# Performance work log

Hardware: AMD Instinct MI355X
Metric: run time of the kernel (lower is better)

## Reference

```python
import jax, jax.numpy as jnp
import numpy as np

N, K, C_IN, H, W = 32, 17, 2048, 64, 64
POSEMB, HID, NLAYERS = 64, 128, 4
IMG = jnp.array([1920.0, 1080.0, 1920.0, 1080.0], jnp.float32)  # image_width/height from img_metas
# H36M 17-joint skeleton edges
EDGES = [(0,1),(1,2),(2,3),(0,4),(4,5),(5,6),(0,7),(7,8),(8,9),(9,10),(8,11),(11,12),(12,13),(8,14),(14,15),(15,16)]
_m = np.eye(K, dtype=bool)
for _i, _j in EDGES:
    _m[_i, _j] = _m[_j, _i] = True
ADJ_MASK = jnp.asarray(_m)
EYE = jnp.eye(K, dtype=jnp.float32)
BN_EPS = 1e-5


def semgconv(x, Wp, b, E):
    # SemGraphConv: separate weights for self (W[0]) and neighbor (W[1]) paths,
    # learned edge logits E masked to the skeleton and row-softmaxed.
    h0 = jnp.einsum('bkc,cd->bkd', x, Wp[0])
    h1 = jnp.einsum('bkc,cd->bkd', x, Wp[1])
    adj = jax.nn.softmax(jnp.where(ADJ_MASK, E, -9e15), axis=1)
    return (jnp.einsum('ij,bjd->bid', adj * EYE, h0)
            + jnp.einsum('ij,bjd->bid', adj * (1.0 - EYE), h1) + b)


def bn_relu(x, gamma, beta):
    # BatchNorm1d in eval mode with running_mean=0, running_var=1, then ReLU.
    return jax.nn.relu(x * gamma * jax.lax.rsqrt(jnp.float32(1.0 + BN_EPS)) + beta)


def setup_inputs() -> dict:
    key = jax.random.key(0)
    ks = jax.random.split(key, 12)
    C_emb = POSEMB + C_IN  # 2112
    NG = 2 * NLAYERS       # 8 hidden graph convs (4 residual blocks x 2)
    return {
        'x': jax.random.normal(ks[0], (N, C_IN, H, W), jnp.float32),
        'heatmap': jax.random.uniform(ks[1], (N, K, H, W), jnp.float32),
        'bbox': jax.random.uniform(ks[2], (N, 4), jnp.float32) * IMG,
        'pos_w': jax.random.normal(ks[3], (6, POSEMB), jnp.float32) * 0.2,
        'pos_b': jnp.zeros((POSEMB,), jnp.float32),
        'Wi': jax.random.normal(ks[4], (2, C_emb, HID), jnp.float32) * 0.02,
        'bi': jnp.zeros((HID,), jnp.float32),
        'Ei': jax.random.normal(ks[5], (K, K), jnp.float32),
        'gi': jnp.ones((HID,), jnp.float32),
        'bti': jnp.zeros((HID,), jnp.float32),
        'Wh': jax.random.normal(ks[6], (NG, 2, HID, HID), jnp.float32) * 0.05,
        'bh': jnp.zeros((NG, HID), jnp.float32),
        'Eh': jax.random.normal(ks[7], (NG, K, K), jnp.float32),
        'gh': jnp.ones((NG, HID), jnp.float32),
        'bth': jnp.zeros((NG, HID), jnp.float32),
        'Wo': jax.random.normal(ks[8], (2, HID, 3), jnp.float32) * 0.05,
        'bo': jnp.zeros((3,), jnp.float32),
        'Eo': jax.random.normal(ks[9], (K, K), jnp.float32),
    }


def reference(x, heatmap, bbox, pos_w, pos_b, Wi, bi, Ei, gi, bti, Wh, bh, Eh, gh, bth, Wo, bo, Eo):
    # get_keypoint: argmax over flattened heatmap -> (kx, ky), normalized to [-1,1]
    loc = jnp.argmax(heatmap.reshape(N, K, H * W), axis=2)          # [N,K] flat index ky*W+kx
    kx = (loc % W).astype(jnp.float32)
    ky = (loc // W).astype(jnp.float32)
    kp = jnp.stack([kx / W * 2.0 - 1.0, ky / H * 2.0 - 1.0], axis=-1)  # [N,K,2]
    # get_bbox: normalize by image size, first two coords -> [-1,1], broadcast over K
    bnrm = bbox / IMG
    bnrm = jnp.concatenate([bnrm[:, :2] * 2.0 - 1.0, bnrm[:, 2:]], axis=1)
    bb = jnp.broadcast_to(bnrm[:, None, :], (N, K, 4))
    # posemb MLP (single Linear(6, 64) since posemb_dim=[64])
    posemb = jnp.concatenate([kp, bb], axis=2) @ pos_w + pos_b      # [N,K,64]
    # featemb: vectorized replacement of the per-(i,j) Python-loop gather x[i,:,ky,kx]
    featemb = jnp.take_along_axis(x.reshape(N, C_IN, H * W), loc[:, None, :], axis=2)
    featemb = featemb.transpose(0, 2, 1)                            # [N,K,2048]
    h = jnp.concatenate([posemb, featemb], axis=2)                  # [N,K,2112]
    # SemGCN: input gconv + BN + ReLU, 4 residual blocks, output gconv
    h = bn_relu(semgconv(h, Wi, bi, Ei), gi, bti)
    for l in range(NLAYERS):
        r = h
        for s in range(2):
            i = 2 * l + s
            r = bn_relu(semgconv(r, Wh[i], bh[i], Eh[i]), gh[i], bth[i])
        h = h + r
    return semgconv(h, Wo, bo, Eo)                                  # [N,K,3]
```

## Files before the change

kernel.cpp:

```cpp
#include <hip/hip_runtime.h>

#define NB    32
#define KJ    17
#define CIN   2048
#define HWSZ  4096
#define WDIM  64
#define CEMB  2112
#define HID   128
#define NROWS (NB*KJ)
#define SPLITK 4

__device__ __constant__ unsigned c_mask[KJ] = {
  0x00093u, 0x00007u, 0x0000Eu, 0x0000Cu, 0x00031u, 0x00070u, 0x00060u,
  0x00181u, 0x04B80u, 0x00700u, 0x00600u, 0x01900u, 0x03800u, 0x03000u,
  0x0C100u, 0x1C000u, 0x18000u
};

__device__ __forceinline__ float fma4(const float4 s, const float4 wv, float a) {
  return fmaf(s.x, wv.x, fmaf(s.y, wv.y, fmaf(s.z, wv.z, fmaf(s.w, wv.w, a))));
}

__global__ __launch_bounds__(256) void k_front(
    const float* __restrict__ heatmap, const float* __restrict__ bbox,
    const float* __restrict__ pos_w, const float* __restrict__ pos_b,
    const float* __restrict__ Wi, const float* __restrict__ Wh,
    const float* __restrict__ x, float* __restrict__ h_ws,
    float4* __restrict__ Wpi4, float4* __restrict__ Wph4) {
  const int blk = blockIdx.x;
  const int t = threadIdx.x;

  if (blk >= NROWS) {
    const int pb = blk - NROWS;
    if (pb < 528) {
      const int idx4 = pb * 256 + t;
      const int d = idx4 & 127, rest = idx4 >> 7;
      const int c4 = rest % 528, p = rest / 528;
      const float* src = Wi + ((size_t)(p * CEMB + c4 * 4)) * HID + d;
      Wpi4[((size_t)p * 528 + c4) * 128 + d] =
          make_float4(src[0], src[HID], src[2 * HID], src[3 * HID]);
    } else {
      const int idx4 = (pb - 528) * 256 + t;
      const int d = idx4 & 127, rest = idx4 >> 7;
      const int c4 = rest & 31, lp = rest >> 5;
      const float* src = Wh + ((size_t)(lp * HID + c4 * 4)) * HID + d;
      Wph4[((size_t)lp * 32 + c4) * 128 + d] =
          make_float4(src[0], src[HID], src[2 * HID], src[3 * HID]);
    }
    return;
  }

  const int b = blk;
  const int n = b / KJ;
  __shared__ float svals[256];
  __shared__ int   sidx[256];

  const float4* hm4 = (const float4*)(heatmap + (size_t)b * HWSZ);
  float best = -1e30f; int bidx = 0;
  #pragma unroll
  for (int k = 0; k < 4; ++k) {
    const int vi = k * 256 + t;
    const float4 v = hm4[vi];
    const int base = vi * 4;
    if (v.x > best) { best = v.x; bidx = base;     }
    if (v.y > best) { best = v.y; bidx = base + 1; }
    if (v.z > best) { best = v.z; bidx = base + 2; }
    if (v.w > best) { best = v.w; bidx = base + 3; }
  }
  svals[t] = best; sidx[t] = bidx;
  __syncthreads();
  for (int s = 128; s > 0; s >>= 1) {
    if (t < s) {
      const float v2 = svals[t + s]; const int i2 = sidx[t + s];
      if (v2 > svals[t] || (v2 == svals[t] && i2 < sidx[t])) {
        svals[t] = v2; sidx[t] = i2;
      }
    }
    __syncthreads();
  }
  const int loc = sidx[0];

  if (t < 64) {
    const float kx = (float)(loc & (WDIM - 1));
    const float ky = (float)(loc >> 6);
    float in6[6];
    in6[0] = kx * (2.0f / 64.0f) - 1.0f;
    in6[1] = ky * (2.0f / 64.0f) - 1.0f;
    in6[2] = bbox[n * 4 + 0] * (2.0f / 1920.0f) - 1.0f;
    in6[3] = bbox[n * 4 + 1] * (2.0f / 1080.0f) - 1.0f;
    in6[4] = bbox[n * 4 + 2] * (1.0f / 1920.0f);
    in6[5] = bbox[n * 4 + 3] * (1.0f / 1080.0f);
    float acc = pos_b[t];
    #pragma unroll
    for (int c = 0; c < 6; ++c) acc = fmaf(in6[c], pos_w[c * 64 + t], acc);
    h_ws[(size_t)b * CEMB + t] = acc;
  }

  const float* xn = x + (size_t)n * CIN * HWSZ + loc;
  float* hrow = h_ws + (size_t)b * CEMB + 64;
  #pragma unroll
  for (int k = 0; k < 8; ++k) {
    const int c = k * 256 + t;
    hrow[c] = xn[(size_t)c * HWSZ];
  }
}

__global__ __launch_bounds__(256) void k_gemm_in(
    const float* __restrict__ Wpi_f, const float* __restrict__ h_ws,
    float* __restrict__ part) {
  const int bm = blockIdx.x, bn = blockIdx.y, bz = blockIdx.z;
  const int t = threadIdx.x;
  const int lane = t & 63, g = t >> 6;
  const int j = bn * 64 + lane;
  const int p = j >> 7, d = j & 127;
  const int row0 = bm * 16;

  const float4* W4 = (const float4*)Wpi_f + ((size_t)p * 528 + bz * 132) * 128 + d;
  const int k0 = bz * 528;

  __shared__ float At[16][48];
  float acc[4] = {0.f, 0.f, 0.f, 0.f};
  float4 ws[3];

  ws[0] = W4[0];
  ws[1] = W4[128];

  for (int st = 0; st < 11; ++st) {
    const int kk = k0 + st * 48;
    __syncthreads();
    for (int idx = t; idx < 16 * 48; idx += 256) {
      const int r = idx / 48, c = idx - r * 48;
      At[r][c] = h_ws[(size_t)(row0 + r) * CEMB + kk + c];
    }
    __syncthreads();
    #pragma unroll
    for (int u = 0; u < 12; ++u) {
      {
        int pf = st * 12 + u + 2;
        pf = pf < 132 ? pf : 131;
        ws[(u + 2) % 3] = W4[(size_t)pf * 128];
      }
      const float4 wv = ws[u % 3];
      #pragma unroll
      for (int r = 0; r < 4; ++r) {
        const float4 s = *(const float4*)&At[g * 4 + r][u * 4];
        acc[r] = fma4(s, wv, acc[r]);
      }
    }
  }
  #pragma unroll
  for (int r = 0; r < 4; ++r) {
    part[((size_t)bz * NROWS + row0 + g * 4 + r) * 256 + j] = acc[r];
  }
}

__device__ __forceinline__ void layer_p(
    const float (*S)[HID], const float4* __restrict__ Wp,
    float (*Op)[HID], int r0, int j) {
  float a[5] = {0.f, 0.f, 0.f, 0.f, 0.f};
  float4 ws[4];
  ws[0] = Wp[j]; ws[1] = Wp[128 + j]; ws[2] = Wp[256 + j];
  #pragma unroll
  for (int cc = 0; cc < 32; ++cc) {
    if (cc < 29) ws[(cc + 3) % 4] = Wp[(cc + 3) * 128 + j];
    const float4 wv = ws[cc % 4];
    #pragma unroll
    for (int r = 0; r < 5; ++r)
      a[r] = fma4(*(const float4*)&S[r0 + r][cc * 4], wv, a[r]);
  }
  #pragma unroll
  for (int r = 0; r < 5; ++r) Op[r0 + r][j] = a[r];
}

template <int ADD>
__device__ __forceinline__ void mix_bn2(
    const float (*T0)[HID], const float (*T1)[HID], const float (*A)[KJ],
    float pb, float pg, float pt, float (*dst)[HID], int g, int d) {
  const float gsv = pg * 0.99999500003749969f;
  for (int i = g; i < KJ; i += 8) {
    float s = 0.f;
    #pragma unroll
    for (int jj = 0; jj < KJ; ++jj) s = fmaf(A[i][jj], T1[jj][d], s);
    s += A[i][i] * (T0[i][d] - T1[i][d]);
    const float v = fmaxf(fmaf(s + pb, gsv, pt), 0.f);
    if (ADD) dst[i][d] += v; else dst[i][d] = v;
  }
}

__global__ __launch_bounds__(1024) void k_gcn(
    const float* __restrict__ part,
    const float* __restrict__ Ei, const float* __restrict__ bi,
    const float* __restrict__ gi, const float* __restrict__ bti,
    const float* __restrict__ Wph, const float* __restrict__ bh,
    const float* __restrict__ Eh, const float* __restrict__ gh,
    const float* __restrict__ bth, const float* __restrict__ Wo,
    const float* __restrict__ bo, const float* __restrict__ Eo,
    float* __restrict__ out) {
  __shared__ float adjm[10][KJ][KJ];
  __shared__ float Hs[20][HID], Rs[20][HID], T0s[20][HID], T1s[20][HID];
  const int n = blockIdx.x, t = threadIdx.x;
  const int p = t >> 9;
  const int qq = (t >> 7) & 3;
  const int j = t & 127;
  const int g = t >> 7;
  const int r0 = qq * 5;

  const float ibb = bi[j], igg = gi[j], ibt = bti[j];
  float pbh[8], pgh[8], pth[8];
  #pragma unroll
  for (int i = 0; i < 8; ++i) {
    pbh[i] = bh[i * HID + j]; pgh[i] = gh[i * HID + j]; pth[i] = bth[i * HID + j];
  }

  if (t < 170) {
    const int m = t / KJ, i = t % KJ;
    const float* Es = (m == 0) ? Ei : ((m <= 8) ? Eh + (size_t)(m - 1) * KJ * KJ : Eo);
    const unsigned msk = c_mask[i];
    float mx = -1e30f;
    #pragma unroll
    for (int jj = 0; jj < KJ; ++jj)
      if (msk & (1u << jj)) mx = fmaxf(mx, Es[i * KJ + jj]);
    float ev[KJ];
    float sum = 0.f;
    #pragma unroll
    for (int jj = 0; jj < KJ; ++jj) {
      const float e = (msk & (1u << jj)) ? expf(Es[i * KJ + jj] - mx) : 0.f;
      ev[jj] = e; sum += e;
    }
    const float inv = 1.f / sum;
    #pragma unroll
    for (int jj = 0; jj < KJ; ++jj) adjm[m][i][jj] = ev[jj] * inv;
  }
  if (t < 384) { Hs[17 + (t >> 7)][t & 127] = 0.f; Rs[17 + (t >> 7)][t & 127] = 0.f; }

  {
    const float* p0 = part + (size_t)(n * KJ) * 256;
    for (int idx = t; idx < KJ * 256; idx += 1024) {
      const int k = idx >> 8, jj = idx & 255;
      float v = 0.f;
      #pragma unroll
      for (int z = 0; z < SPLITK; ++z)
        v += p0[(size_t)z * NROWS * 256 + k * 256 + jj];
      if (jj < HID) T0s[k][jj] = v; else T1s[k][jj - HID] = v;
    }
  }
  __syncthreads();

  mix_bn2<0>(T0s, T1s, adjm[0], ibb, igg, ibt, Hs, g, j);
  __syncthreads();

  const float4* Wp4 = (const float4*)Wph;
  for (int l = 0; l < 4; ++l) {
    const int iA = 2 * l, iB = 2 * l + 1;
    layer_p(Hs, Wp4 + (size_t)(iA * 2 + p) * 4096, p ? T1s : T0s, r0, j);
    __syncthreads();
    mix_bn2<0>(T0s, T1s, adjm[1 + iA], pbh[iA], pgh[iA], pth[iA], Rs, g, j);
    __syncthreads();
    layer_p(Rs, Wp4 + (size_t)(iB * 2 + p) * 4096, p ? T1s : T0s, r0, j);
    __syncthreads();
    mix_bn2<1>(T0s, T1s, adjm[1 + iB], pbh[iB], pgh[iB], pth[iB], Hs, g, j);
    __syncthreads();
  }

  if (t < 102) {
    const int pp = t / 51, rem = t % 51, i = rem / 3, e = rem % 3;
    const float* Wp = Wo + pp * HID * 3 + e;
    float s = 0.f;
    #pragma unroll 4
    for (int c = 0; c < HID; ++c) s = fmaf(Hs[i][c], Wp[c * 3], s);
    if (pp == 0) T0s[i][e] = s; else T1s[i][e] = s;
  }
  __syncthreads();
  if (t < 51) {
    const int i = t / 3, e = t % 3;
    const float (*A)[KJ] = adjm[9];
    float s = bo[e];
    #pragma unroll
    for (int jj = 0; jj < KJ; ++jj) s = fmaf(A[i][jj], T1s[jj][e], s);
    s += A[i][i] * (T0s[i][e] - T1s[i][e]);
    out[(n * KJ + i) * 3 + e] = s;
  }
}

extern "C" void kernel_launch(void* const* d_in, const int* in_sizes, int n_in,
                              void* d_out, int out_size, void* d_ws, size_t ws_size,
                              hipStream_t stream) {
  const float* x       = (const float*)d_in[0];
  const float* heatmap = (const float*)d_in[1];
  const float* bbox    = (const float*)d_in[2];
  const float* pos_w   = (const float*)d_in[3];
  const float* pos_b   = (const float*)d_in[4];
  const float* Wi      = (const float*)d_in[5];
  const float* bi      = (const float*)d_in[6];
  const float* Ei      = (const float*)d_in[7];
  const float* gi      = (const float*)d_in[8];
  const float* bti     = (const float*)d_in[9];
  const float* Wh      = (const float*)d_in[10];
  const float* bh      = (const float*)d_in[11];
  const float* Eh      = (const float*)d_in[12];
  const float* gh      = (const float*)d_in[13];
  const float* bth     = (const float*)d_in[14];
  const float* Wo      = (const float*)d_in[15];
  const float* bo      = (const float*)d_in[16];
  const float* Eo      = (const float*)d_in[17];
  float* out = (float*)d_out;

  float* h_ws = (float*)d_ws;
  float* part = h_ws + (size_t)NROWS * CEMB;
  float* Wpi  = part + (size_t)SPLITK * NROWS * 256;
  float* Wph  = Wpi + (size_t)2 * CEMB * HID;

  k_front<<<NROWS + 528 + 256, 256, 0, stream>>>(
      heatmap, bbox, pos_w, pos_b, Wi, Wh, x, h_ws,
      (float4*)Wpi, (float4*)Wph);
  k_gemm_in<<<dim3(34, 4, SPLITK), 256, 0, stream>>>(Wpi, h_ws, part);
  k_gcn<<<NB, 1024, 0, stream>>>(part, Ei, bi, gi, bti, Wph, bh, Eh, gh, bth,
                                 Wo, bo, Eo, out);
}
```

Measured before the change: 148.8 us.

## Stage hidden-layer weights in LDS and halve GCN block to 512 threads

The hidden SemGCN layers now run with 512 threads per block instead of 1024. Each thread computes both self and neighbor paths in sequence. Before each path, the block cooperatively copies that path's 128x128 weight matrix into shared memory, and every thread then reads its weight float4 from LDS rather than from global memory with a software prefetch. The neighbor weights are loaded into registers early so the second global load can overlap the first path's compute. In exchange the kernel gains 64KB of LDS, extra barriers and half the threads, so per-thread work doubles on a kernel that only launches 32 blocks.

```diff
diff --git a/kernel.cpp b/kernel.cpp
--- a/kernel.cpp
+++ b/kernel.cpp
@@ -153,30 +153,27 @@
   }
 }
 
-__device__ __forceinline__ void layer_p(
-    const float (*S)[HID], const float4* __restrict__ Wp,
-    float (*Op)[HID], int r0, int j) {
+__device__ __forceinline__ void compute_path(
+    const float (*S)[HID], const float4* __restrict__ Wlds,
+    float (*T)[HID], int r0, int j) {
   float a[5] = {0.f, 0.f, 0.f, 0.f, 0.f};
-  float4 ws[4];
-  ws[0] = Wp[j]; ws[1] = Wp[128 + j]; ws[2] = Wp[256 + j];
   #pragma unroll
   for (int cc = 0; cc < 32; ++cc) {
-    if (cc < 29) ws[(cc + 3) % 4] = Wp[(cc + 3) * 128 + j];
-    const float4 wv = ws[cc % 4];
+    const float4 wv = Wlds[cc * 128 + j];
     #pragma unroll
     for (int r = 0; r < 5; ++r)
       a[r] = fma4(*(const float4*)&S[r0 + r][cc * 4], wv, a[r]);
   }
   #pragma unroll
-  for (int r = 0; r < 5; ++r) Op[r0 + r][j] = a[r];
+  for (int r = 0; r < 5; ++r) T[r0 + r][j] = a[r];
 }
 
 template <int ADD>
 __device__ __forceinline__ void mix_bn2(
     const float (*T0)[HID], const float (*T1)[HID], const float (*A)[KJ],
-    float pb, float pg, float pt, float (*dst)[HID], int g, int d) {
+    float pb, float pg, float pt, float (*dst)[HID], int q, int d) {
   const float gsv = pg * 0.99999500003749969f;
-  for (int i = g; i < KJ; i += 8) {
+  for (int i = q; i < KJ; i += 4) {
     float s = 0.f;
     #pragma unroll
     for (int jj = 0; jj < KJ; ++jj) s = fmaf(A[i][jj], T1[jj][d], s);
@@ -186,7 +183,7 @@
   }
 }
 
-__global__ __launch_bounds__(1024) void k_gcn(
+__global__ __launch_bounds__(512) void k_gcn(
     const float* __restrict__ part,
     const float* __restrict__ Ei, const float* __restrict__ bi,
     const float* __restrict__ gi, const float* __restrict__ bti,
@@ -197,19 +194,12 @@
     float* __restrict__ out) {
   __shared__ float adjm[10][KJ][KJ];
   __shared__ float Hs[20][HID], Rs[20][HID], T0s[20][HID], T1s[20][HID];
+  __shared__ float4 Wlds[32 * 128];
   const int n = blockIdx.x, t = threadIdx.x;
-  const int p = t >> 9;
-  const int qq = (t >> 7) & 3;
-  const int j = t & 127;
-  const int g = t >> 7;
-  const int r0 = qq * 5;
+  const int q = t >> 7, j = t & 127;
+  const int r0 = q * 5;
 
   const float ibb = bi[j], igg = gi[j], ibt = bti[j];
-  float pbh[8], pgh[8], pth[8];
-  #pragma unroll
-  for (int i = 0; i < 8; ++i) {
-    pbh[i] = bh[i * HID + j]; pgh[i] = gh[i * HID + j]; pth[i] = bth[i * HID + j];
-  }
 
   if (t < 170) {
     const int m = t / KJ, i = t % KJ;
@@ -234,7 +224,7 @@
 
   {
     const float* p0 = part + (size_t)(n * KJ) * 256;
-    for (int idx = t; idx < KJ * 256; idx += 1024) {
+    for (int idx = t; idx < KJ * 256; idx += 512) {
       const int k = idx >> 8, jj = idx & 255;
       float v = 0.f;
       #pragma unroll
@@ -245,20 +235,40 @@
   }
   __syncthreads();
 
-  mix_bn2<0>(T0s, T1s, adjm[0], ibb, igg, ibt, Hs, g, j);
+  mix_bn2<0>(T0s, T1s, adjm[0], ibb, igg, ibt, Hs, q, j);
   __syncthreads();
 
   const float4* Wp4 = (const float4*)Wph;
   for (int l = 0; l < 4; ++l) {
-    const int iA = 2 * l, iB = 2 * l + 1;
-    layer_p(Hs, Wp4 + (size_t)(iA * 2 + p) * 4096, p ? T1s : T0s, r0, j);
-    __syncthreads();
-    mix_bn2<0>(T0s, T1s, adjm[1 + iA], pbh[iA], pgh[iA], pth[iA], Rs, g, j);
-    __syncthreads();
-    layer_p(Rs, Wp4 + (size_t)(iB * 2 + p) * 4096, p ? T1s : T0s, r0, j);
-    __syncthreads();
-    mix_bn2<1>(T0s, T1s, adjm[1 + iB], pbh[iB], pgh[iB], pth[iB], Hs, g, j);
-    __syncthreads();
+    #pragma unroll
+    for (int s = 0; s < 2; ++s) {
+      const int il = 2 * l + s;
+      const float pb = bh[il * HID + j], pg = gh[il * HID + j], pt = bth[il * HID + j];
+      const float4* W0g = Wp4 + (size_t)(il * 2) * 4096;
+      const float4* W1g = W0g + 4096;
+      const float (*S)[HID] = (s == 0) ? Hs : Rs;
+
+      float4 w1r[8];
+      #pragma unroll
+      for (int u = 0; u < 8; ++u) w1r[u] = W1g[u * 512 + t];
+      #pragma unroll
+      for (int u = 0; u < 8; ++u) Wlds[u * 512 + t] = W0g[u * 512 + t];
+      __syncthreads();
+      compute_path(S, Wlds, T0s, r0, j);
+      __syncthreads();
+      #pragma unroll
+      for (int u = 0; u < 8; ++u) Wlds[u * 512 + t] = w1r[u];
+      __syncthreads();
+      compute_path(S, Wlds, T1s, r0, j);
+      __syncthreads();
+
+      if (s == 0) {
+        mix_bn2<0>(T0s, T1s, adjm[1 + il], pb, pg, pt, Rs, q, j);
+      } else {
+        mix_bn2<1>(T0s, T1s, adjm[1 + il], pb, pg, pt, Hs, q, j);
+      }
+      __syncthreads();
+    }
   }
 
   if (t < 102) {
@@ -313,6 +323,6 @@
       heatmap, bbox, pos_w, pos_b, Wi, Wh, x, h_ws,
       (float4*)Wpi, (float4*)Wph);
   k_gemm_in<<<dim3(34, 4, SPLITK), 256, 0, stream>>>(Wpi, h_ws, part);
-  k_gcn<<<NB, 1024, 0, stream>>>(part, Ei, bi, gi, bti, Wph, bh, Eh, gh, bth,
-                                 Wo, bo, Eo, out);
-}
+  k_gcn<<<NB, 512, 0, stream>>>(part, Ei, bi, gi, bti, Wph, bh, Eh, gh, bth,
+                                Wo, bo, Eo, out);
+}
```

Result: slower. 173.7 us (+16.7%).
